# Performance work log

Hardware: AMD Instinct MI355X
Metric: run time of the kernel (lower is better)

The kernel has to match this reference:

```python
import jax, jax.numpy as jnp
import numpy as np

N_NODES = 50000
N_EDGES = 800000
D_FEAT = 128
UNITS = 128
N_HOPS = 3  # K + 1 with K = 2


def setup_inputs() -> dict:
    key = jax.random.key(0)
    k1, k2, k3, k4, k5 = jax.random.split(key, 5)
    x = jax.random.normal(k1, (N_NODES, D_FEAT), dtype=jnp.float32)
    kernel = jax.random.normal(k2, (N_HOPS, D_FEAT, UNITS), dtype=jnp.float32) * 0.05
    bias = jax.random.normal(k3, (N_HOPS, UNITS), dtype=jnp.float32) * 0.05
    edge_weight = jax.random.uniform(k4, (N_HOPS, N_EDGES), dtype=jnp.float32)
    edge_index = jax.random.randint(k5, (N_HOPS, 2, N_EDGES), 0, N_NODES, dtype=jnp.int64)
    return {"x": x, "kernel": kernel, "bias": bias,
            "edge_weight": edge_weight, "edge_index": edge_index}


def reference(x, kernel, bias, edge_weight, edge_index):
    # output = relu( sum_i  adj_i @ (x @ W_i) + b_i )
    n = x.shape[0]
    out = jnp.zeros((n, kernel.shape[-1]), dtype=x.dtype)
    for i in range(kernel.shape[0]):  # small fixed loop over K+1 hops
        h = x @ kernel[i]                                  # [N, units] dense projection
        src, dst = edge_index[i, 0], edge_index[i, 1]
        msg = h[src] * edge_weight[i][:, None]             # [E, units] weighted gather
        agg = jax.ops.segment_sum(msg, dst, num_segments=n)  # SpMM via scatter-add
        out = out + agg + bias[i]
    return jax.nn.relu(out)
```

## Files before the change

kernel.cpp:

```cpp
#include <hip/hip_runtime.h>

#define NN 50000
#define DD 128
#define EE 800000
#define NHOPS 3
#define CAP 64

typedef unsigned short u16;
typedef __attribute__((ext_vector_type(8))) short short8v;
typedef __attribute__((ext_vector_type(8))) unsigned short ushort8v;
typedef __attribute__((ext_vector_type(4))) float f32x4;

__device__ inline u16 f2bf(float f) {
    unsigned u = __float_as_uint(f);
    unsigned r = u + 0x7FFFu + ((u >> 16) & 1u);
    return (u16)(r >> 16);
}

__global__ __launch_bounds__(256) void prep_x_kernel(const float* __restrict__ x,
                                                     u16* __restrict__ xb) {
    int i = blockIdx.x * 256 + threadIdx.x;
    if (i < NN * DD / 4) {
        float4 v = *(const float4*)(x + (size_t)i * 4);
        ushort4 o = make_ushort4(f2bf(v.x), f2bf(v.y), f2bf(v.z), f2bf(v.w));
        *(ushort4*)(xb + (size_t)i * 4) = o;
    }
}
__global__ __launch_bounds__(256) void prep_w_kernel(const float* __restrict__ W,
                                                     u16* __restrict__ Wt) {
    int i = blockIdx.x * 256 + threadIdx.x;
    if (i < NHOPS * DD * DD) {
        int hop = i / (DD * DD);
        int rem = i - hop * DD * DD;
        int k = rem >> 7, c = rem & (DD - 1);
        Wt[(size_t)hop * DD * DD + c * DD + k] = f2bf(W[i]);
    }
}

__global__ __launch_bounds__(256) void gemm_mfma_kernel(const u16* __restrict__ xb,
                                                        const u16* __restrict__ Wt,
                                                        u16* __restrict__ h) {
    __shared__ u16 xs[64][136];
    __shared__ u16 ws[128][136];
    const int tid  = threadIdx.x;
    const int row0 = blockIdx.x * 64;

    for (int i = tid; i < 1024; i += 256) {
        int r = i >> 4, c8 = (i & 15) * 8;
        int gr = row0 + r;
        ushort8v v = {0, 0, 0, 0, 0, 0, 0, 0};
        if (gr < NN) v = *(const ushort8v*)(xb + (size_t)gr * DD + c8);
        *(ushort8v*)&xs[r][c8] = v;
    }
    for (int i = tid; i < 2048; i += 256) {
        int r = i >> 4, c8 = (i & 15) * 8;
        *(ushort8v*)&ws[r][c8] = *(const ushort8v*)(Wt + (size_t)r * DD + c8);
    }
    __syncthreads();

    const int wv = tid >> 6;
    const int l  = tid & 63;
    const int lr = l & 15;
    const int lk = (l >> 4) * 8;

    f32x4 acc[8] = {};
    #pragma unroll
    for (int kb = 0; kb < 4; ++kb) {
        short8v a = *(const short8v*)&xs[wv * 16 + lr][kb * 32 + lk];
        #pragma unroll
        for (int ct = 0; ct < 8; ++ct) {
            short8v b = *(const short8v*)&ws[ct * 16 + lr][kb * 32 + lk];
            acc[ct] = __builtin_amdgcn_mfma_f32_16x16x32_bf16(a, b, acc[ct], 0, 0, 0);
        }
    }

    const int orow = wv * 16 + (l >> 4) * 4;
    #pragma unroll
    for (int ct = 0; ct < 8; ++ct) {
        #pragma unroll
        for (int j = 0; j < 4; ++j) {
            int gr = row0 + orow + j;
            if (gr < NN) h[(size_t)gr * DD + ct * 16 + lr] = f2bf(acc[ct][j]);
        }
    }
}

__global__ __launch_bounds__(256) void fill_kernel(const int* __restrict__ dst,
                                                   int* __restrict__ cnt,
                                                   int* __restrict__ bucket) {
    int e = blockIdx.x * 256 + threadIdx.x;
    if (e >= EE) return;
    int d = dst[e];
    int slot = atomicAdd(&cnt[d], 1);
    if (slot < CAP) bucket[d * CAP + slot] = e;
}

template<int MODE>
__global__ __launch_bounds__(256) void spmm_kernel(const u16* __restrict__ h,
                                                   const int* __restrict__ src,
                                                   const float* __restrict__ ew,
                                                   const int* __restrict__ bucket,
                                                   const int* __restrict__ cnt,
                                                   const float* __restrict__ bias,
                                                   float* __restrict__ out) {
    const int wave = (blockIdx.x * 256 + threadIdx.x) >> 6;
    const int lane = threadIdx.x & 63;
    if (wave >= NN) return;

    const int half = lane >> 5;
    const int hl   = lane & 31;
    const int c0   = hl * 4;

    const int deg = cnt[wave];
    const int nb  = deg < CAP ? deg : CAP;

    int   s = 0;
    float w = 0.f;
    if (lane < nb) {
        int eid = bucket[wave * CAP + lane];
        s = src[eid];
        w = ew[eid];
    }

    float a0 = 0.f, a1 = 0.f, a2 = 0.f, a3 = 0.f;
    for (int t = 0; t < nb; t += 2) {
        int   idx = t + half;
        int   sj  = __shfl(s, idx);
        float wj  = __shfl(w, idx);
        uint2 v   = *(const uint2*)(h + (size_t)sj * DD + c0);
        a0 = fmaf(wj, __uint_as_float(v.x << 16),        a0);
        a1 = fmaf(wj, __uint_as_float(v.x & 0xFFFF0000u), a1);
        a2 = fmaf(wj, __uint_as_float(v.y << 16),        a2);
        a3 = fmaf(wj, __uint_as_float(v.y & 0xFFFF0000u), a3);
    }

    a0 += __shfl_xor(a0, 32);
    a1 += __shfl_xor(a1, 32);
    a2 += __shfl_xor(a2, 32);
    a3 += __shfl_xor(a3, 32);

    if (half == 0) {
        float* op = out + (size_t)wave * DD + c0;
        float4 p;
        if (MODE == 0) {
            float4 b0 = *(const float4*)(bias + c0);
            float4 b1 = *(const float4*)(bias + DD + c0);
            float4 b2 = *(const float4*)(bias + 2 * DD + c0);
            p = make_float4(b0.x + b1.x + b2.x + a0,
                            b0.y + b1.y + b2.y + a1,
                            b0.z + b1.z + b2.z + a2,
                            b0.w + b1.w + b2.w + a3);
        } else {
            float4 prev = *(const float4*)op;
            p = make_float4(prev.x + a0, prev.y + a1, prev.z + a2, prev.w + a3);
            if (MODE == 2) {
                p.x = fmaxf(p.x, 0.f); p.y = fmaxf(p.y, 0.f);
                p.z = fmaxf(p.z, 0.f); p.w = fmaxf(p.w, 0.f);
            }
        }
        *(float4*)op = p;
    }
}

extern "C" void kernel_launch(void* const* d_in, const int* in_sizes, int n_in,
                              void* d_out, int out_size, void* d_ws, size_t ws_size,
                              hipStream_t stream) {
    const float* x       = (const float*)d_in[0];
    const float* kernels = (const float*)d_in[1];
    const float* bias    = (const float*)d_in[2];
    const float* ew      = (const float*)d_in[3];
    const int*   eidx    = (const int*)d_in[4];
    float* out = (float*)d_out;

    u16* xb     = (u16*)d_ws;
    u16* hbuf   = xb + (size_t)NN * DD;
    int* bucket = (int*)(hbuf + (size_t)NN * DD);
    int* cnt    = bucket + (size_t)NN * CAP;
    u16* Wt     = (u16*)(cnt + NN);

    const int px_blocks   = (NN * DD / 4) / 256;
    const int pw_blocks   = (NHOPS * DD * DD + 255) / 256;
    const int gemm_blocks = (NN + 63) / 64;
    const int fill_blocks = (EE + 255) / 256;
    const int spmm_blocks = (NN * 64) / 256;

    prep_x_kernel<<<px_blocks, 256, 0, stream>>>(x, xb);
    prep_w_kernel<<<pw_blocks, 256, 0, stream>>>(kernels, Wt);

    for (int i = 0; i < NHOPS; ++i) {
        const int*   src_i = eidx + (size_t)i * 2 * EE;
        const int*   dst_i = src_i + EE;
        const float* ew_i  = ew + (size_t)i * EE;

        gemm_mfma_kernel<<<gemm_blocks, 256, 0, stream>>>(xb, Wt + (size_t)i * DD * DD, hbuf);
        hipMemsetAsync(cnt, 0, NN * sizeof(int), stream);
        fill_kernel<<<fill_blocks, 256, 0, stream>>>(dst_i, cnt, bucket);
        if (i == 0)
            spmm_kernel<0><<<spmm_blocks, 256, 0, stream>>>(hbuf, src_i, ew_i, bucket, cnt, bias, out);
        else if (i == 1)
            spmm_kernel<1><<<spmm_blocks, 256, 0, stream>>>(hbuf, src_i, ew_i, bucket, cnt, bias, out);
        else
            spmm_kernel<2><<<spmm_blocks, 256, 0, stream>>>(hbuf, src_i, ew_i, bucket, cnt, bias, out);
    }
}
```

Baseline: 462.0 us.

## Fuse x bf16 conversion into GEMM, vectorize fill, unroll SpMM, single memset

Removes the separate x-to-bf16 prep kernel and converts fp32 x to bf16 while loading tiles in the GEMM, at the cost of reading fp32 x once per hop. The fill kernel now handles four edges per thread with an int4 load, and the SpMM gather loop is unrolled to keep two neighbor loads in flight. Per-hop counter memsets become one memset over three separate count arrays. Together these cut launch count and raise memory-level parallelism, but the GEMM now reads twice as many bytes of x on every hop.

Result: faster. 438.0 us (-5.2%).

```diff
diff --git a/kernel.cpp b/kernel.cpp
--- a/kernel.cpp
+++ b/kernel.cpp
@@ -17,15 +17,6 @@
     return (u16)(r >> 16);
 }
 
-__global__ __launch_bounds__(256) void prep_x_kernel(const float* __restrict__ x,
-                                                     u16* __restrict__ xb) {
-    int i = blockIdx.x * 256 + threadIdx.x;
-    if (i < NN * DD / 4) {
-        float4 v = *(const float4*)(x + (size_t)i * 4);
-        ushort4 o = make_ushort4(f2bf(v.x), f2bf(v.y), f2bf(v.z), f2bf(v.w));
-        *(ushort4*)(xb + (size_t)i * 4) = o;
-    }
-}
 __global__ __launch_bounds__(256) void prep_w_kernel(const float* __restrict__ W,
                                                      u16* __restrict__ Wt) {
     int i = blockIdx.x * 256 + threadIdx.x;
@@ -37,7 +28,7 @@
     }
 }
 
-__global__ __launch_bounds__(256) void gemm_mfma_kernel(const u16* __restrict__ xb,
+__global__ __launch_bounds__(256) void gemm_mfma_kernel(const float* __restrict__ x,
                                                         const u16* __restrict__ Wt,
                                                         u16* __restrict__ h) {
     __shared__ u16 xs[64][136];
@@ -45,12 +36,13 @@
     const int tid  = threadIdx.x;
     const int row0 = blockIdx.x * 64;
 
-    for (int i = tid; i < 1024; i += 256) {
-        int r = i >> 4, c8 = (i & 15) * 8;
+    for (int i = tid; i < 2048; i += 256) {
+        int r = i >> 5, c4 = (i & 31) * 4;
         int gr = row0 + r;
-        ushort8v v = {0, 0, 0, 0, 0, 0, 0, 0};
-        if (gr < NN) v = *(const ushort8v*)(xb + (size_t)gr * DD + c8);
-        *(ushort8v*)&xs[r][c8] = v;
+        float4 v = make_float4(0.f, 0.f, 0.f, 0.f);
+        if (gr < NN) v = *(const float4*)(x + (size_t)gr * DD + c4);
+        ushort4 o = make_ushort4(f2bf(v.x), f2bf(v.y), f2bf(v.z), f2bf(v.w));
+        *(ushort4*)&xs[r][c4] = o;
     }
     for (int i = tid; i < 2048; i += 256) {
         int r = i >> 4, c8 = (i & 15) * 8;
@@ -88,11 +80,18 @@
 __global__ __launch_bounds__(256) void fill_kernel(const int* __restrict__ dst,
                                                    int* __restrict__ cnt,
                                                    int* __restrict__ bucket) {
-    int e = blockIdx.x * 256 + threadIdx.x;
-    if (e >= EE) return;
-    int d = dst[e];
-    int slot = atomicAdd(&cnt[d], 1);
-    if (slot < CAP) bucket[d * CAP + slot] = e;
+    int t = blockIdx.x * 256 + threadIdx.x;
+    if (t >= EE / 4) return;
+    int e0 = t * 4;
+    int4 d = *(const int4*)(dst + e0);
+    int s0 = atomicAdd(&cnt[d.x], 1);
+    int s1 = atomicAdd(&cnt[d.y], 1);
+    int s2 = atomicAdd(&cnt[d.z], 1);
+    int s3 = atomicAdd(&cnt[d.w], 1);
+    if (s0 < CAP) bucket[d.x * CAP + s0] = e0;
+    if (s1 < CAP) bucket[d.y * CAP + s1] = e0 + 1;
+    if (s2 < CAP) bucket[d.z * CAP + s2] = e0 + 2;
+    if (s3 < CAP) bucket[d.w * CAP + s3] = e0 + 3;
 }
 
 template<int MODE>
@@ -123,14 +122,30 @@
     }
 
     float a0 = 0.f, a1 = 0.f, a2 = 0.f, a3 = 0.f;
-    for (int t = 0; t < nb; t += 2) {
+    int t = 0;
+    for (; t + 4 <= nb; t += 4) {
+        int   iA = t + half,      iB = t + 2 + half;
+        int   sA = __shfl(s, iA); int   sB = __shfl(s, iB);
+        float wA = __shfl(w, iA); float wB = __shfl(w, iB);
+        uint2 vA = *(const uint2*)(h + (size_t)sA * DD + c0);
+        uint2 vB = *(const uint2*)(h + (size_t)sB * DD + c0);
+        a0 = fmaf(wA, __uint_as_float(vA.x << 16),         a0);
+        a1 = fmaf(wA, __uint_as_float(vA.x & 0xFFFF0000u), a1);
+        a2 = fmaf(wA, __uint_as_float(vA.y << 16),         a2);
+        a3 = fmaf(wA, __uint_as_float(vA.y & 0xFFFF0000u), a3);
+        a0 = fmaf(wB, __uint_as_float(vB.x << 16),         a0);
+        a1 = fmaf(wB, __uint_as_float(vB.x & 0xFFFF0000u), a1);
+        a2 = fmaf(wB, __uint_as_float(vB.y << 16),         a2);
+        a3 = fmaf(wB, __uint_as_float(vB.y & 0xFFFF0000u), a3);
+    }
+    for (; t < nb; t += 2) {
         int   idx = t + half;
         int   sj  = __shfl(s, idx);
         float wj  = __shfl(w, idx);
         uint2 v   = *(const uint2*)(h + (size_t)sj * DD + c0);
-        a0 = fmaf(wj, __uint_as_float(v.x << 16),        a0);
+        a0 = fmaf(wj, __uint_as_float(v.x << 16),         a0);
         a1 = fmaf(wj, __uint_as_float(v.x & 0xFFFF0000u), a1);
-        a2 = fmaf(wj, __uint_as_float(v.y << 16),        a2);
+        a2 = fmaf(wj, __uint_as_float(v.y << 16),         a2);
         a3 = fmaf(wj, __uint_as_float(v.y & 0xFFFF0000u), a3);
     }
 
@@ -172,34 +187,32 @@
     const int*   eidx    = (const int*)d_in[4];
     float* out = (float*)d_out;
 
-    u16* xb     = (u16*)d_ws;
-    u16* hbuf   = xb + (size_t)NN * DD;
+    u16* hbuf   = (u16*)d_ws;
     int* bucket = (int*)(hbuf + (size_t)NN * DD);
     int* cnt    = bucket + (size_t)NN * CAP;
-    u16* Wt     = (u16*)(cnt + NN);
-
-    const int px_blocks   = (NN * DD / 4) / 256;
+    u16* Wt     = (u16*)(cnt + (size_t)NHOPS * NN);
+
     const int pw_blocks   = (NHOPS * DD * DD + 255) / 256;
     const int gemm_blocks = (NN + 63) / 64;
-    const int fill_blocks = (EE + 255) / 256;
+    const int fill_blocks = (EE / 4 + 255) / 256;
     const int spmm_blocks = (NN * 64) / 256;
 
-    prep_x_kernel<<<px_blocks, 256, 0, stream>>>(x, xb);
     prep_w_kernel<<<pw_blocks, 256, 0, stream>>>(kernels, Wt);
+    hipMemsetAsync(cnt, 0, (size_t)NHOPS * NN * sizeof(int), stream);
 
     for (int i = 0; i < NHOPS; ++i) {
         const int*   src_i = eidx + (size_t)i * 2 * EE;
         const int*   dst_i = src_i + EE;
         const float* ew_i  = ew + (size_t)i * EE;
-
-        gemm_mfma_kernel<<<gemm_blocks, 256, 0, stream>>>(xb, Wt + (size_t)i * DD * DD, hbuf);
-        hipMemsetAsync(cnt, 0, NN * sizeof(int), stream);
-        fill_kernel<<<fill_blocks, 256, 0, stream>>>(dst_i, cnt, bucket);
+        int*         cnt_i = cnt + (size_t)i * NN;
+
+        gemm_mfma_kernel<<<gemm_blocks, 256, 0, stream>>>(x, Wt + (size_t)i * DD * DD, hbuf);
+        fill_kernel<<<fill_blocks, 256, 0, stream>>>(dst_i, cnt_i, bucket);
         if (i == 0)
-            spmm_kernel<0><<<spmm_blocks, 256, 0, stream>>>(hbuf, src_i, ew_i, bucket, cnt, bias, out);
+            spmm_kernel<0><<<spmm_blocks, 256, 0, stream>>>(hbuf, src_i, ew_i, bucket, cnt_i, bias, out);
         else if (i == 1)
-            spmm_kernel<1><<<spmm_blocks, 256, 0, stream>>>(hbuf, src_i, ew_i, bucket, cnt, bias, out);
+            spmm_kernel<1><<<spmm_blocks, 256, 0, stream>>>(hbuf, src_i, ew_i, bucket, cnt_i, bias, out);
         else
-            spmm_kernel<2><<<spmm_blocks, 256, 0, stream>>>(hbuf, src_i, ew_i, bucket, cnt, bias, out);
-    }
-}
+            spmm_kernel<2><<<spmm_blocks, 256, 0, stream>>>(hbuf, src_i, ew_i, bucket, cnt_i, bias, out);
+    }
+}
```
